# Performance work log

Hardware: AMD Instinct MI355X
Metric: run time of the kernel (lower is better)

The kernel has to match this reference:

```python
import jax, jax.numpy as jnp
import numpy as np

N = 8192
IN_F = 512
OUT_F = 256
POW = 2


def setup_inputs() -> dict:
    key = jax.random.key(0)
    k1, k2, k3, k4 = jax.random.split(key, 4)
    stdv = 1.0 / np.sqrt(OUT_F)
    inputs = {
        "input": jax.random.normal(k1, (N, IN_F), dtype=jnp.float32),
        "adj": jax.random.uniform(k2, (N, N), dtype=jnp.float32),
        "weight": jax.random.uniform(k3, (IN_F, OUT_F), dtype=jnp.float32, minval=-stdv, maxval=stdv),
        "bias": jax.random.uniform(k4, (OUT_F,), dtype=jnp.float32, minval=-stdv, maxval=stdv),
    }
    return inputs


def reference(input, adj, weight, bias):
    # K_adj = adj ** pow (elementwise power, as torch's ** on a dense tensor)
    k_adj = adj ** POW
    # support = X @ W  -> [N, out_features]
    support = jnp.einsum("ni,io->no", input, weight)
    # output = K_adj @ support -> [N, out_features]
    out = jnp.einsum("nm,mo->no", k_adj, support) + bias
    # F.elu with default alpha=1.0
    return jnp.where(out > 0, out, jnp.expm1(out))
```

## Files before the change

kernel.cpp:

```cpp
#include <hip/hip_runtime.h>
#include <cstdint>
#include <cstddef>

#define N_NODES 8192
#define INF 512
#define OUTF 256
#define SPLITK 8
#define MSLICE (N_NODES / SPLITK)
#define BN2 128

typedef _Float16 f16;
typedef _Float16 f16x8 __attribute__((ext_vector_type(8)));
typedef _Float16 f16x4 __attribute__((ext_vector_type(4)));
typedef float f32x4 __attribute__((ext_vector_type(4)));

__device__ __forceinline__ void async_copy16(void* lds_dst, const void* g_src) {
  __builtin_amdgcn_global_load_lds(
      (const __attribute__((address_space(1))) void*)g_src,
      (__attribute__((address_space(3))) void*)lds_dst,
      16, 0, 0);
}

__device__ __forceinline__ float elu(float x) { return x > 0.f ? x : expm1f(x); }

__global__ __launch_bounds__(256) void prep_w(const float* __restrict__ W,
                                              f16* __restrict__ WhT) {
  const int idx = blockIdx.x * 256 + threadIdx.x;
  const int o = idx >> 9, i = idx & 511;
  WhT[idx] = (f16)W[i * OUTF + o];
}

__global__ __launch_bounds__(256) void gemm1(const f16* __restrict__ WhT,
                                             const float* __restrict__ X,
                                             f16* __restrict__ supT) {
  __shared__ __align__(16) f16 Asm[64 * 64];
  __shared__ __align__(16) f16 Bsm[64 * 64];
  const int t = threadIdx.x;
  const int wave = t >> 6, lane = t & 63;
  const int q = lane >> 4, r = lane & 15;
  const int lrow = lane >> 3, lchunk = lane & 7;
  const int o0 = blockIdx.x * 64, m0 = blockIdx.y * 64;

  f32x4 acc[4];
#pragma unroll
  for (int i = 0; i < 4; ++i) acc[i] = (f32x4){0.f, 0.f, 0.f, 0.f};

  const int b_row = t >> 2;
  const int b_c0 = (t & 3) * 2;
  const float* xptr = X + (size_t)(m0 + b_row) * INF + (t & 3) * 16;

  for (int kt = 0; kt < 8; ++kt) {
    const int k0 = kt * 64;
#pragma unroll
    for (int op = 0; op < 2; ++op) {
      const int row = (wave * 2 + op) * 8 + lrow;
      const f16* src = WhT + (size_t)(o0 + row) * INF + k0 + (lchunk ^ lrow) * 8;
      async_copy16(Asm + (wave * 2 + op) * 512, src);
    }
    {
      const float* xp = xptr + k0;
      f32x4 v0 = *(const f32x4*)(xp + 0);
      f32x4 v1 = *(const f32x4*)(xp + 4);
      f32x4 v2 = *(const f32x4*)(xp + 8);
      f32x4 v3 = *(const f32x4*)(xp + 12);
      f16x8 h0, h1;
#pragma unroll
      for (int u = 0; u < 4; ++u) {
        h0[u] = (f16)v0[u];
        h0[4 + u] = (f16)v1[u];
        h1[u] = (f16)v2[u];
        h1[4 + u] = (f16)v3[u];
      }
      *(f16x8*)&Bsm[b_row * 64 + ((b_c0 ^ (b_row & 7)) * 8)] = h0;
      *(f16x8*)&Bsm[b_row * 64 + (((b_c0 + 1) ^ (b_row & 7)) * 8)] = h1;
    }
    __syncthreads();
#pragma unroll
    for (int s = 0; s < 2; ++s) {
      const int pc = ((s * 4 + q) ^ (r & 7)) * 8;
      f16x8 af[4];
#pragma unroll
      for (int i = 0; i < 4; ++i) af[i] = *(const f16x8*)&Asm[(i * 16 + r) * 64 + pc];
      const f16x8 bf = *(const f16x8*)&Bsm[(wave * 16 + r) * 64 + pc];
#pragma unroll
      for (int i = 0; i < 4; ++i)
        acc[i] = __builtin_amdgcn_mfma_f32_16x16x32_f16(af[i], bf, acc[i], 0, 0, 0);
    }
    __syncthreads();
  }
  const int m = m0 + wave * 16 + r;
#pragma unroll
  for (int i = 0; i < 4; ++i)
#pragma unroll
    for (int g = 0; g < 4; ++g)
      supT[(size_t)(o0 + i * 16 + q * 4 + g) * N_NODES + m] = (f16)acc[i][g];
}

template <bool ATOMIC>
__global__ __launch_bounds__(512, 4) void gemm2(const float* __restrict__ adj,
                                                const f16* __restrict__ supT,
                                                f16* __restrict__ P16,
                                                float* __restrict__ outp) {
  __shared__ __align__(16) f16 Asm[BN2 * 64];
  __shared__ __align__(16) f16 Bsm[256 * 64];
  const int t = threadIdx.x;
  const int wave = t >> 6, lane = t & 63;
  const int q = lane >> 4, r = lane & 15;
  const int wn = wave >> 2, wo = wave & 3;
  const int wg = blockIdx.x;
  const int y = wg & 7;
  const int n0 = (wg >> 3) * BN2;
  const size_t m_base = (size_t)y * MSLICE;

  f32x4 acc[4][4];
#pragma unroll
  for (int i = 0; i < 4; ++i)
#pragma unroll
    for (int j = 0; j < 4; ++j) acc[i][j] = (f32x4){0.f, 0.f, 0.f, 0.f};

  const int a_row = t >> 2;
  const int a_c0 = (t & 3) * 2;
  const float* aptr = adj + (size_t)(n0 + a_row) * N_NODES + m_base + (t & 3) * 16;
  const int b_o8 = lane >> 3;
  const int b_kb = lane & 7;

  for (int kt = 0; kt < MSLICE / 64; ++kt) {
#pragma unroll
    for (int j = 0; j < 4; ++j) {
      const int c = wave * 4 + j;
      const int o = c * 8 + b_o8;
      const int kb = b_kb ^ (o & 7);
      const f16* src = supT + (size_t)o * N_NODES + m_base + kt * 64 + kb * 8;
      async_copy16(Bsm + c * 8 * 64, src);
    }
    {
      const float* ap = aptr + kt * 64;
      f32x4 v0 = *(const f32x4*)(ap + 0);
      f32x4 v1 = *(const f32x4*)(ap + 4);
      f32x4 v2 = *(const f32x4*)(ap + 8);
      f32x4 v3 = *(const f32x4*)(ap + 12);
      f16x8 h0, h1;
#pragma unroll
      for (int u = 0; u < 4; ++u) {
        h0[u] = (f16)(v0[u] * v0[u]);
        h0[4 + u] = (f16)(v1[u] * v1[u]);
        h1[u] = (f16)(v2[u] * v2[u]);
        h1[4 + u] = (f16)(v3[u] * v3[u]);
      }
      *(f16x8*)&Asm[a_row * 64 + ((a_c0 ^ (a_row & 7)) * 8)] = h0;
      *(f16x8*)&Asm[a_row * 64 + (((a_c0 + 1) ^ (a_row & 7)) * 8)] = h1;
    }
    __syncthreads();
#pragma unroll
    for (int s = 0; s < 2; ++s) {
      const int pc = ((s * 4 + q) ^ (r & 7)) * 8;
      f16x8 af[4], bf[4];
#pragma unroll
      for (int i = 0; i < 4; ++i)
        af[i] = *(const f16x8*)&Asm[(wn * 64 + i * 16 + r) * 64 + pc];
#pragma unroll
      for (int j = 0; j < 4; ++j)
        bf[j] = *(const f16x8*)&Bsm[(wo * 64 + j * 16 + r) * 64 + pc];
#pragma unroll
      for (int i = 0; i < 4; ++i)
#pragma unroll
        for (int j = 0; j < 4; ++j)
          acc[i][j] = __builtin_amdgcn_mfma_f32_16x16x32_f16(af[i], bf[j],
                                                             acc[i][j], 0, 0, 0);
    }
    __syncthreads();
  }
  if (ATOMIC) {
#pragma unroll
    for (int i = 0; i < 4; ++i)
#pragma unroll
      for (int g = 0; g < 4; ++g) {
        const int n = n0 + wn * 64 + i * 16 + q * 4 + g;
        float* orow = outp + (size_t)n * OUTF + wo * 64 + r;
#pragma unroll
        for (int j = 0; j < 4; ++j) atomicAdd(orow + j * 16, acc[i][j][g]);
      }
  } else {
    f16* base = P16 + (size_t)y * N_NODES * OUTF;
#pragma unroll
    for (int i = 0; i < 4; ++i)
#pragma unroll
      for (int g = 0; g < 4; ++g) {
        const int n = n0 + wn * 64 + i * 16 + q * 4 + g;
        f16* orow = base + (size_t)n * OUTF + wo * 64 + r;
#pragma unroll
        for (int j = 0; j < 4; ++j) orow[j * 16] = (f16)acc[i][j][g];
      }
  }
}

__global__ __launch_bounds__(256) void reduce_elu(const f16* __restrict__ P16,
                                                  const float* __restrict__ bias,
                                                  float* __restrict__ out) {
  const int idx = blockIdx.x * 256 + threadIdx.x;
  float s[8];
#pragma unroll
  for (int u = 0; u < 8; ++u) s[u] = 0.f;
#pragma unroll
  for (int y = 0; y < SPLITK; ++y) {
    const f16x8 h = ((const f16x8*)(P16 + (size_t)y * N_NODES * OUTF))[idx];
#pragma unroll
    for (int u = 0; u < 8; ++u) s[u] += (float)h[u];
  }
  const float* bp = bias + (idx & 31) * 8;
  f32x4 v0, v1;
#pragma unroll
  for (int u = 0; u < 4; ++u) {
    v0[u] = elu(s[u] + bp[u]);
    v1[u] = elu(s[4 + u] + bp[4 + u]);
  }
  ((f32x4*)out)[idx * 2 + 0] = v0;
  ((f32x4*)out)[idx * 2 + 1] = v1;
}

__global__ __launch_bounds__(256) void bias_elu(float* __restrict__ out,
                                                const float* __restrict__ bias) {
  const int idx = blockIdx.x * 256 + threadIdx.x;
  f32x4 v = ((const f32x4*)out)[idx];
  const f32x4 b = ((const f32x4*)bias)[idx & 63];
#pragma unroll
  for (int u = 0; u < 4; ++u) v[u] = elu(v[u] + b[u]);
  ((f32x4*)out)[idx] = v;
}

extern "C" void kernel_launch(void* const* d_in, const int* in_sizes, int n_in,
                              void* d_out, int out_size, void* d_ws, size_t ws_size,
                              hipStream_t stream) {
  const float* X = (const float*)d_in[0];
  const float* adj = (const float*)d_in[1];
  const float* W = (const float*)d_in[2];
  const float* bias = (const float*)d_in[3];
  float* out = (float*)d_out;

  char* ws = (char*)d_ws;
  f16* supT = (f16*)(ws + 0);
  f16* WhT = (f16*)(ws + (4u << 20));
  f16* P16 = (f16*)(ws + (8u << 20));
  const size_t need = (40u << 20);

  prep_w<<<INF * OUTF / 256, 256, 0, stream>>>(W, WhT);
  gemm1<<<dim3(OUTF / 64, N_NODES / 64), 256, 0, stream>>>(WhT, X, supT);
  if (ws_size >= need) {
    gemm2<false><<<dim3((N_NODES / BN2) * SPLITK), dim3(512), 0, stream>>>(adj, supT, P16, nullptr);
    reduce_elu<<<N_NODES * OUTF / 8 / 256, 256, 0, stream>>>(P16, bias, out);
  } else {
    hipMemsetAsync(d_out, 0, (size_t)out_size * sizeof(float), stream);
    gemm2<true><<<dim3((N_NODES / BN2) * SPLITK), dim3(512), 0, stream>>>(adj, supT, nullptr, out);
    bias_elu<<<N_NODES * OUTF / 4 / 256, 256, 0, stream>>>(out, bias);
  }
}
```

Baseline: 417.9 us.

## Double-buffer LDS in both GEMMs and halve split-K to 4

Both GEMM kernels now use two LDS buffers, issuing async loads and register prefetch for the next k-tile while MFMAs run on the current one, with one barrier per iteration. gemm2 also drops split-K from 8 to 4, which halves the fp16 partial buffer and the reduce traffic but doubles the per-block K loop and halves the grid to 256 blocks. The launch-bounds occupancy hint is removed and LDS per block doubles (about 96KB for gemm2), so fewer blocks fit per CU, reducing latency hiding across waves.

```diff
diff --git a/kernel.cpp b/kernel.cpp
--- a/kernel.cpp
+++ b/kernel.cpp
@@ -5,9 +5,11 @@
 #define N_NODES 8192
 #define INF 512
 #define OUTF 256
-#define SPLITK 8
+#define SPLITK 4
+#define LOG_SPLITK 2
 #define MSLICE (N_NODES / SPLITK)
 #define BN2 128
+#define KT2 (MSLICE / 64)
 
 typedef _Float16 f16;
 typedef _Float16 f16x8 __attribute__((ext_vector_type(8)));
@@ -33,8 +35,8 @@
 __global__ __launch_bounds__(256) void gemm1(const f16* __restrict__ WhT,
                                              const float* __restrict__ X,
                                              f16* __restrict__ supT) {
-  __shared__ __align__(16) f16 Asm[64 * 64];
-  __shared__ __align__(16) f16 Bsm[64 * 64];
+  __shared__ __align__(16) f16 Asm[2][64 * 64];
+  __shared__ __align__(16) f16 Bsm[2][64 * 64];
   const int t = threadIdx.x;
   const int wave = t >> 6, lane = t & 63;
   const int q = lane >> 4, r = lane & 15;
@@ -49,43 +51,59 @@
   const int b_c0 = (t & 3) * 2;
   const float* xptr = X + (size_t)(m0 + b_row) * INF + (t & 3) * 16;
 
-  for (int kt = 0; kt < 8; ++kt) {
-    const int k0 = kt * 64;
+  f32x4 xv[4];
+
+  auto issueA = [&](int kt, int buf) {
 #pragma unroll
     for (int op = 0; op < 2; ++op) {
       const int row = (wave * 2 + op) * 8 + lrow;
-      const f16* src = WhT + (size_t)(o0 + row) * INF + k0 + (lchunk ^ lrow) * 8;
-      async_copy16(Asm + (wave * 2 + op) * 512, src);
-    }
-    {
-      const float* xp = xptr + k0;
-      f32x4 v0 = *(const f32x4*)(xp + 0);
-      f32x4 v1 = *(const f32x4*)(xp + 4);
-      f32x4 v2 = *(const f32x4*)(xp + 8);
-      f32x4 v3 = *(const f32x4*)(xp + 12);
-      f16x8 h0, h1;
-#pragma unroll
-      for (int u = 0; u < 4; ++u) {
-        h0[u] = (f16)v0[u];
-        h0[4 + u] = (f16)v1[u];
-        h1[u] = (f16)v2[u];
-        h1[4 + u] = (f16)v3[u];
-      }
-      *(f16x8*)&Bsm[b_row * 64 + ((b_c0 ^ (b_row & 7)) * 8)] = h0;
-      *(f16x8*)&Bsm[b_row * 64 + (((b_c0 + 1) ^ (b_row & 7)) * 8)] = h1;
-    }
-    __syncthreads();
+      const f16* src = WhT + (size_t)(o0 + row) * INF + kt * 64 + (lchunk ^ lrow) * 8;
+      async_copy16(&Asm[buf][(wave * 2 + op) * 512], src);
+    }
+  };
+  auto loadB = [&](int kt) {
+    const float* xp = xptr + kt * 64;
+    xv[0] = *(const f32x4*)(xp + 0);
+    xv[1] = *(const f32x4*)(xp + 4);
+    xv[2] = *(const f32x4*)(xp + 8);
+    xv[3] = *(const f32x4*)(xp + 12);
+  };
+  auto writeB = [&](int buf) {
+    f16x8 h0, h1;
+#pragma unroll
+    for (int u = 0; u < 4; ++u) {
+      h0[u] = (f16)xv[0][u];
+      h0[4 + u] = (f16)xv[1][u];
+      h1[u] = (f16)xv[2][u];
+      h1[4 + u] = (f16)xv[3][u];
+    }
+    *(f16x8*)&Bsm[buf][b_row * 64 + ((b_c0 ^ (b_row & 7)) * 8)] = h0;
+    *(f16x8*)&Bsm[buf][b_row * 64 + (((b_c0 + 1) ^ (b_row & 7)) * 8)] = h1;
+  };
+
+  issueA(0, 0);
+  loadB(0);
+  writeB(0);
+  __syncthreads();
+
+  for (int kt = 0; kt < 8; ++kt) {
+    const int c = kt & 1, o = c ^ 1;
+    if (kt + 1 < 8) {
+      issueA(kt + 1, o);
+      loadB(kt + 1);
+    }
 #pragma unroll
     for (int s = 0; s < 2; ++s) {
       const int pc = ((s * 4 + q) ^ (r & 7)) * 8;
       f16x8 af[4];
 #pragma unroll
-      for (int i = 0; i < 4; ++i) af[i] = *(const f16x8*)&Asm[(i * 16 + r) * 64 + pc];
-      const f16x8 bf = *(const f16x8*)&Bsm[(wave * 16 + r) * 64 + pc];
+      for (int i = 0; i < 4; ++i) af[i] = *(const f16x8*)&Asm[c][(i * 16 + r) * 64 + pc];
+      const f16x8 bf = *(const f16x8*)&Bsm[c][(wave * 16 + r) * 64 + pc];
 #pragma unroll
       for (int i = 0; i < 4; ++i)
         acc[i] = __builtin_amdgcn_mfma_f32_16x16x32_f16(af[i], bf, acc[i], 0, 0, 0);
     }
+    if (kt + 1 < 8) writeB(o);
     __syncthreads();
   }
   const int m = m0 + wave * 16 + r;
@@ -97,19 +115,19 @@
 }
 
 template <bool ATOMIC>
-__global__ __launch_bounds__(512, 4) void gemm2(const float* __restrict__ adj,
-                                                const f16* __restrict__ supT,
-                                                f16* __restrict__ P16,
-                                                float* __restrict__ outp) {
-  __shared__ __align__(16) f16 Asm[BN2 * 64];
-  __shared__ __align__(16) f16 Bsm[256 * 64];
+__global__ __launch_bounds__(512) void gemm2(const float* __restrict__ adj,
+                                             const f16* __restrict__ supT,
+                                             f16* __restrict__ P16,
+                                             float* __restrict__ outp) {
+  __shared__ __align__(16) f16 Asm[2][BN2 * 64];
+  __shared__ __align__(16) f16 Bsm[2][256 * 64];
   const int t = threadIdx.x;
   const int wave = t >> 6, lane = t & 63;
   const int q = lane >> 4, r = lane & 15;
   const int wn = wave >> 2, wo = wave & 3;
   const int wg = blockIdx.x;
-  const int y = wg & 7;
-  const int n0 = (wg >> 3) * BN2;
+  const int y = wg & (SPLITK - 1);
+  const int n0 = (wg >> LOG_SPLITK) * BN2;
   const size_t m_base = (size_t)y * MSLICE;
 
   f32x4 acc[4][4];
@@ -124,43 +142,59 @@
   const int b_o8 = lane >> 3;
   const int b_kb = lane & 7;
 
-  for (int kt = 0; kt < MSLICE / 64; ++kt) {
+  f32x4 av[4];
+
+  auto issueB = [&](int kt, int buf) {
 #pragma unroll
     for (int j = 0; j < 4; ++j) {
       const int c = wave * 4 + j;
       const int o = c * 8 + b_o8;
       const int kb = b_kb ^ (o & 7);
       const f16* src = supT + (size_t)o * N_NODES + m_base + kt * 64 + kb * 8;
-      async_copy16(Bsm + c * 8 * 64, src);
-    }
-    {
-      const float* ap = aptr + kt * 64;
-      f32x4 v0 = *(const f32x4*)(ap + 0);
-      f32x4 v1 = *(const f32x4*)(ap + 4);
-      f32x4 v2 = *(const f32x4*)(ap + 8);
-      f32x4 v3 = *(const f32x4*)(ap + 12);
-      f16x8 h0, h1;
-#pragma unroll
-      for (int u = 0; u < 4; ++u) {
-        h0[u] = (f16)(v0[u] * v0[u]);
-        h0[4 + u] = (f16)(v1[u] * v1[u]);
-        h1[u] = (f16)(v2[u] * v2[u]);
-        h1[4 + u] = (f16)(v3[u] * v3[u]);
-      }
-      *(f16x8*)&Asm[a_row * 64 + ((a_c0 ^ (a_row & 7)) * 8)] = h0;
-      *(f16x8*)&Asm[a_row * 64 + (((a_c0 + 1) ^ (a_row & 7)) * 8)] = h1;
-    }
-    __syncthreads();
+      async_copy16(&Bsm[buf][c * 8 * 64], src);
+    }
+  };
+  auto loadA = [&](int kt) {
+    const float* ap = aptr + kt * 64;
+    av[0] = *(const f32x4*)(ap + 0);
+    av[1] = *(const f32x4*)(ap + 4);
+    av[2] = *(const f32x4*)(ap + 8);
+    av[3] = *(const f32x4*)(ap + 12);
+  };
+  auto writeA = [&](int buf) {
+    f16x8 h0, h1;
+#pragma unroll
+    for (int u = 0; u < 4; ++u) {
+      h0[u] = (f16)(av[0][u] * av[0][u]);
+      h0[4 + u] = (f16)(av[1][u] * av[1][u]);
+      h1[u] = (f16)(av[2][u] * av[2][u]);
+      h1[4 + u] = (f16)(av[3][u] * av[3][u]);
+    }
+    *(f16x8*)&Asm[buf][a_row * 64 + ((a_c0 ^ (a_row & 7)) * 8)] = h0;
+    *(f16x8*)&Asm[buf][a_row * 64 + (((a_c0 + 1) ^ (a_row & 7)) * 8)] = h1;
+  };
+
+  issueB(0, 0);
+  loadA(0);
+  writeA(0);
+  __syncthreads();
+
+  for (int kt = 0; kt < KT2; ++kt) {
+    const int cb = kt & 1, ob = cb ^ 1;
+    if (kt + 1 < KT2) {
+      issueB(kt + 1, ob);
+      loadA(kt + 1);
+    }
 #pragma unroll
     for (int s = 0; s < 2; ++s) {
       const int pc = ((s * 4 + q) ^ (r & 7)) * 8;
       f16x8 af[4], bf[4];
 #pragma unroll
       for (int i = 0; i < 4; ++i)
-        af[i] = *(const f16x8*)&Asm[(wn * 64 + i * 16 + r) * 64 + pc];
+        af[i] = *(const f16x8*)&Asm[cb][(wn * 64 + i * 16 + r) * 64 + pc];
 #pragma unroll
       for (int j = 0; j < 4; ++j)
-        bf[j] = *(const f16x8*)&Bsm[(wo * 64 + j * 16 + r) * 64 + pc];
+        bf[j] = *(const f16x8*)&Bsm[cb][(wo * 64 + j * 16 + r) * 64 + pc];
 #pragma unroll
       for (int i = 0; i < 4; ++i)
 #pragma unroll
@@ -168,6 +202,7 @@
           acc[i][j] = __builtin_amdgcn_mfma_f32_16x16x32_f16(af[i], bf[j],
                                                              acc[i][j], 0, 0, 0);
     }
+    if (kt + 1 < KT2) writeA(ob);
     __syncthreads();
   }
   if (ATOMIC) {
@@ -241,7 +276,7 @@
   f16* supT = (f16*)(ws + 0);
   f16* WhT = (f16*)(ws + (4u << 20));
   f16* P16 = (f16*)(ws + (8u << 20));
-  const size_t need = (40u << 20);
+  const size_t need = (32u << 20);
 
   prep_w<<<INF * OUTF / 256, 256, 0, stream>>>(W, WhT);
   gemm1<<<dim3(OUTF / 64, N_NODES / 64), 256, 0, stream>>>(WhT, X, supT);
```

Result: slower. 432.3 us (+3.4%).

## Fuse split-K reduction and ELU into gemm2 via last-block counters

Applied to the files above, without the earlier changes.

The separate reduce_elu launch is replaced: each gemm2 block writes its f16 partial, bumps a per-row-block atomic counter, and the last of the SPLITK blocks for that row block sums the partials, adds bias and applies ELU. The adj loads also become nontemporal so the streamed 256 MB matrix does not pollute the caches. The aim is to drop one kernel launch and let the reduction overlap with other blocks' GEMM work, at the cost of a memset for the counters, thread fences, and tail work concentrated in the last-arriving blocks.

```diff
diff --git a/kernel.cpp b/kernel.cpp
--- a/kernel.cpp
+++ b/kernel.cpp
@@ -6,8 +6,10 @@
 #define INF 512
 #define OUTF 256
 #define SPLITK 8
+#define LOG_SPLITK 3
 #define MSLICE (N_NODES / SPLITK)
 #define BN2 128
+#define KT2 (MSLICE / 64)
 
 typedef _Float16 f16;
 typedef _Float16 f16x8 __attribute__((ext_vector_type(8)));
@@ -100,16 +102,20 @@
 __global__ __launch_bounds__(512, 4) void gemm2(const float* __restrict__ adj,
                                                 const f16* __restrict__ supT,
                                                 f16* __restrict__ P16,
-                                                float* __restrict__ outp) {
+                                                const float* __restrict__ bias,
+                                                float* __restrict__ out,
+                                                int* __restrict__ counters) {
   __shared__ __align__(16) f16 Asm[BN2 * 64];
   __shared__ __align__(16) f16 Bsm[256 * 64];
+  __shared__ int s_last;
   const int t = threadIdx.x;
   const int wave = t >> 6, lane = t & 63;
   const int q = lane >> 4, r = lane & 15;
   const int wn = wave >> 2, wo = wave & 3;
   const int wg = blockIdx.x;
-  const int y = wg & 7;
-  const int n0 = (wg >> 3) * BN2;
+  const int y = wg & (SPLITK - 1);
+  const int nb = wg >> LOG_SPLITK;
+  const int n0 = nb * BN2;
   const size_t m_base = (size_t)y * MSLICE;
 
   f32x4 acc[4][4];
@@ -124,7 +130,7 @@
   const int b_o8 = lane >> 3;
   const int b_kb = lane & 7;
 
-  for (int kt = 0; kt < MSLICE / 64; ++kt) {
+  for (int kt = 0; kt < KT2; ++kt) {
 #pragma unroll
     for (int j = 0; j < 4; ++j) {
       const int c = wave * 4 + j;
@@ -135,10 +141,10 @@
     }
     {
       const float* ap = aptr + kt * 64;
-      f32x4 v0 = *(const f32x4*)(ap + 0);
-      f32x4 v1 = *(const f32x4*)(ap + 4);
-      f32x4 v2 = *(const f32x4*)(ap + 8);
-      f32x4 v3 = *(const f32x4*)(ap + 12);
+      f32x4 v0 = __builtin_nontemporal_load((const f32x4*)(ap + 0));
+      f32x4 v1 = __builtin_nontemporal_load((const f32x4*)(ap + 4));
+      f32x4 v2 = __builtin_nontemporal_load((const f32x4*)(ap + 8));
+      f32x4 v3 = __builtin_nontemporal_load((const f32x4*)(ap + 12));
       f16x8 h0, h1;
 #pragma unroll
       for (int u = 0; u < 4; ++u) {
@@ -170,17 +176,21 @@
     }
     __syncthreads();
   }
+
   if (ATOMIC) {
 #pragma unroll
     for (int i = 0; i < 4; ++i)
 #pragma unroll
       for (int g = 0; g < 4; ++g) {
         const int n = n0 + wn * 64 + i * 16 + q * 4 + g;
-        float* orow = outp + (size_t)n * OUTF + wo * 64 + r;
+        float* orow = out + (size_t)n * OUTF + wo * 64 + r;
 #pragma unroll
         for (int j = 0; j < 4; ++j) atomicAdd(orow + j * 16, acc[i][j][g]);
       }
-  } else {
+    return;
+  }
+
+  {
     f16* base = P16 + (size_t)y * N_NODES * OUTF;
 #pragma unroll
     for (int i = 0; i < 4; ++i)
@@ -192,30 +202,41 @@
         for (int j = 0; j < 4; ++j) orow[j * 16] = (f16)acc[i][j][g];
       }
   }
-}
-
-__global__ __launch_bounds__(256) void reduce_elu(const f16* __restrict__ P16,
-                                                  const float* __restrict__ bias,
-                                                  float* __restrict__ out) {
-  const int idx = blockIdx.x * 256 + threadIdx.x;
-  float s[8];
-#pragma unroll
-  for (int u = 0; u < 8; ++u) s[u] = 0.f;
-#pragma unroll
-  for (int y = 0; y < SPLITK; ++y) {
-    const f16x8 h = ((const f16x8*)(P16 + (size_t)y * N_NODES * OUTF))[idx];
-#pragma unroll
-    for (int u = 0; u < 8; ++u) s[u] += (float)h[u];
-  }
-  const float* bp = bias + (idx & 31) * 8;
-  f32x4 v0, v1;
-#pragma unroll
-  for (int u = 0; u < 4; ++u) {
-    v0[u] = elu(s[u] + bp[u]);
-    v1[u] = elu(s[4 + u] + bp[4 + u]);
-  }
-  ((f32x4*)out)[idx * 2 + 0] = v0;
-  ((f32x4*)out)[idx * 2 + 1] = v1;
+  __syncthreads();
+  if (t == 0) {
+    __threadfence();
+    const int old = atomicAdd(counters + nb, 1);
+    s_last = (old == SPLITK - 1) ? 1 : 0;
+  }
+  __syncthreads();
+  if (s_last == 0) return;
+  __threadfence();
+
+  const f16* pbase = P16 + (size_t)n0 * OUTF;
+  float* obase = out + (size_t)n0 * OUTF;
+#pragma unroll
+  for (int v = 0; v < 8; ++v) {
+    const int idx = v * 512 + t;
+    float s[8];
+#pragma unroll
+    for (int u = 0; u < 8; ++u) s[u] = 0.f;
+#pragma unroll
+    for (int yy = 0; yy < SPLITK; ++yy) {
+      const f16x8 h =
+          ((const f16x8*)(pbase + (size_t)yy * N_NODES * OUTF))[idx];
+#pragma unroll
+      for (int u = 0; u < 8; ++u) s[u] += (float)h[u];
+    }
+    const float* bp = bias + (idx & 31) * 8;
+    f32x4 v0, v1;
+#pragma unroll
+    for (int u = 0; u < 4; ++u) {
+      v0[u] = elu(s[u] + bp[u]);
+      v1[u] = elu(s[4 + u] + bp[4 + u]);
+    }
+    ((f32x4*)obase)[idx * 2 + 0] = v0;
+    ((f32x4*)obase)[idx * 2 + 1] = v1;
+  }
 }
 
 __global__ __launch_bounds__(256) void bias_elu(float* __restrict__ out,
@@ -241,16 +262,19 @@
   f16* supT = (f16*)(ws + 0);
   f16* WhT = (f16*)(ws + (4u << 20));
   f16* P16 = (f16*)(ws + (8u << 20));
-  const size_t need = (40u << 20);
+  int* counters = (int*)(ws + (40u << 20));
+  const size_t need = (40u << 20) + 4096;
 
   prep_w<<<INF * OUTF / 256, 256, 0, stream>>>(W, WhT);
   gemm1<<<dim3(OUTF / 64, N_NODES / 64), 256, 0, stream>>>(WhT, X, supT);
   if (ws_size >= need) {
-    gemm2<false><<<dim3((N_NODES / BN2) * SPLITK), dim3(512), 0, stream>>>(adj, supT, P16, nullptr);
-    reduce_elu<<<N_NODES * OUTF / 8 / 256, 256, 0, stream>>>(P16, bias, out);
+    hipMemsetAsync(counters, 0, 4096, stream);
+    gemm2<false><<<dim3((N_NODES / BN2) * SPLITK), dim3(512), 0, stream>>>(
+        adj, supT, P16, bias, out, counters);
   } else {
     hipMemsetAsync(d_out, 0, (size_t)out_size * sizeof(float), stream);
-    gemm2<true><<<dim3((N_NODES / BN2) * SPLITK), dim3(512), 0, stream>>>(adj, supT, nullptr, out);
+    gemm2<true><<<dim3((N_NODES / BN2) * SPLITK), dim3(512), 0, stream>>>(
+        adj, supT, nullptr, bias, out, nullptr);
     bias_elu<<<N_NODES * OUTF / 4 / 256, 256, 0, stream>>>(out, bias);
   }
 }
```

Measured after the change: 566.8 us. 35.6% more time.
